# Kernel optimization log

Measured on AMD Instinct MI355X. Metric: run time of the kernel, lower is better.

Reference implementation:

```python
import jax, jax.numpy as jnp
import numpy as np

C = 512
GROUPS = 32
EPS = 1e-6

def setup_inputs() -> dict:
    key = jax.random.key(0)
    ks = jax.random.split(key, 8)
    b, h, w = 8, 64, 64
    s = 0.02
    return {
        "x": jax.random.normal(ks[0], (b, C, h, w), dtype=jnp.float32),
        "gn_gamma": jnp.ones((C,), jnp.float32),
        "gn_beta": jnp.zeros((C,), jnp.float32),
        "q_w": jax.random.normal(ks[1], (C, C), jnp.float32) * s,
        "q_b": jnp.zeros((C,), jnp.float32),
        "k_w": jax.random.normal(ks[2], (C, C), jnp.float32) * s,
        "k_b": jnp.zeros((C,), jnp.float32),
        "proj_w": jax.random.normal(ks[3], (C, C), jnp.float32) * s,
        "proj_b": jnp.zeros((C,), jnp.float32),
    }

def _group_norm(x, gamma, beta):
    b, c, h, w = x.shape
    xg = x.reshape(b, GROUPS, c // GROUPS, h, w)
    mu = jnp.mean(xg, axis=(2, 3, 4), keepdims=True)
    var = jnp.var(xg, axis=(2, 3, 4), keepdims=True)
    xn = ((xg - mu) * jax.lax.rsqrt(var + EPS)).reshape(b, c, h, w)
    return xn * gamma[None, :, None, None] + beta[None, :, None, None]

def _conv1x1(x, w, b):
    # x: (b,c,h,w), w: (out,in) -> (b,out,h,w)
    return jnp.einsum('bchw,oc->bohw', x, w) + b[None, :, None, None]

def reference(x, gn_gamma, gn_beta, q_w, q_b, k_w, k_b, proj_w, proj_b):
    b, c, h, w = x.shape
    r = _group_norm(x, gn_gamma, gn_beta)
    q = _conv1x1(r, q_w, q_b).reshape(b, c, h * w)   # (b,c,n)
    k = _conv1x1(r, k_w, k_b).reshape(b, c, h * w)   # (b,c,m)
    v = k  # faithful to source: v = self.k0(r)
    scale = jnp.asarray(c, x.dtype) ** -0.5
    scores = jnp.einsum('bcn,bcm->bnm', q, k) * scale  # (b,n,m)
    attn = jax.nn.softmax(scores, axis=-1)
    out = jnp.einsum('bcm,bnm->bcn', v, attn).reshape(b, c, h, w)
    out = _conv1x1(out, proj_w, proj_b)
    return x + out
```

## Files before the change

### kernel.cpp

```cpp
#include <hip/hip_runtime.h>
#include <hip/hip_bf16.h>
#include <cstdint>

#define DEVI __device__ __forceinline__

typedef __attribute__((ext_vector_type(8))) short short8;
typedef __attribute__((ext_vector_type(4))) float f32x4;
typedef unsigned int u32;
typedef unsigned short u16;

DEVI u16 f2bf(float f) {
  __hip_bfloat16 h = __float2bfloat16(f);
  return *reinterpret_cast<u16*>(&h);
}

DEVI void async_cp16(const __hip_bfloat16* g, __hip_bfloat16* l) {
  __builtin_amdgcn_global_load_lds(
      (const __attribute__((address_space(1))) u32*)(uintptr_t)g,
      (__attribute__((address_space(3))) u32*)(uintptr_t)l, 16, 0, 0);
}

DEVI void xcd_remap(int& bx, int& by, int& bz) {
  const int gx = gridDim.x, gy = gridDim.y;
  const int d = blockIdx.x + gx * (blockIdx.y + gridDim.y * blockIdx.z);
  const int idx = d >> 3;
  const int g = (d & 7) + 8 * (idx / gx);
  bx = idx % gx;
  by = g % gy;
  bz = g / gy;
}


template<int BIAS_MODE, bool EXPSUM>
__global__ __launch_bounds__(512, 2) void gemm256_tn(
    const __hip_bfloat16* __restrict__ A, int lda, size_t sA,
    const __hip_bfloat16* __restrict__ B, int ldb, size_t sB,
    void* __restrict__ Zv, int ldz, size_t sZ,
    const float* __restrict__ bias,
    float alpha, int K,
    float* __restrict__ rsum)
{
  __shared__ __hip_bfloat16 ls[3 * 16384];
  const int t  = threadIdx.x;
  const int bb = blockIdx.z;

  const int nbxy = gridDim.x * gridDim.y;
  const int borig = blockIdx.y * gridDim.x + blockIdx.x;
  const int cpx = nbxy >> 3;
  const int blog = (borig & 7) * cpx + (borig >> 3);
  const int bx = blog % gridDim.x;
  const int by = blog / gridDim.x;
  const int n0 = bx * 256;
  const int m0 = by * 256;

  const __hip_bfloat16* Ab = A + (size_t)bb * sA;
  const __hip_bfloat16* Bb = B + (size_t)bb * sB;

  const int lane = t & 63;
  const int quad = lane >> 4;
  const int l16  = lane & 15;
  const int wave = t >> 6;
  const int wm   = (wave >> 2) * 128;
  const int wn   = (wave & 3) * 64;
  const int qa   = (quad ^ (l16 & 3)) * 8;

  const int rowc = t >> 2;
  const int kc   = ((t & 3) ^ (rowc & 3)) * 8;
  const __hip_bfloat16* ga0 = Ab + (size_t)(m0 + rowc) * lda + kc;
  const __hip_bfloat16* ga1 = Ab + (size_t)(m0 + rowc + 128) * lda + kc;
  const __hip_bfloat16* gb0 = Bb + (size_t)(n0 + rowc) * ldb + kc;
  const __hip_bfloat16* gb1 = Bb + (size_t)(n0 + rowc + 128) * ldb + kc;

  f32x4 acc[8][4] = {};

#define STAGE256(SLOT)                                                        \
  {                                                                           \
    __hip_bfloat16* lb = ls + (SLOT) * 16384 + t * 8;                         \
    async_cp16(ga0, lb);                                                      \
    async_cp16(ga1, lb + 4096);                                               \
    async_cp16(gb0, lb + 8192);                                               \
    async_cp16(gb1, lb + 12288);                                              \
    ga0 += 32; ga1 += 32; gb0 += 32; gb1 += 32;                               \
  }

#define COMPUTE256(SLOT)                                                      \
  {                                                                           \
    const __hip_bfloat16* bA = ls + (SLOT) * 16384;                           \
    const __hip_bfloat16* bB = bA + 8192;                                     \
    short8 af[8], bfr[4];                                                     \
    _Pragma("unroll")                                                         \
    for (int i = 0; i < 8; ++i)                                               \
      af[i] = *(const short8*)(bA + (wm + i * 16 + l16) * 32 + qa);           \
    _Pragma("unroll")                                                         \
    for (int j = 0; j < 4; ++j)                                               \
      bfr[j] = *(const short8*)(bB + (wn + j * 16 + l16) * 32 + qa);          \
    _Pragma("unroll")                                                         \
    for (int i = 0; i < 8; ++i)                                               \
      _Pragma("unroll")                                                       \
      for (int j = 0; j < 4; ++j)                                             \
        acc[i][j] = __builtin_amdgcn_mfma_f32_16x16x32_bf16(af[i], bfr[j],    \
                                                            acc[i][j], 0, 0, 0); \
  }

  STAGE256(0);
  STAGE256(1);
  const int nk = K >> 5;
  for (int kw = 0; kw < nk - 1; ++kw) {
    asm volatile("s_waitcnt vmcnt(4)" ::: "memory");
    __builtin_amdgcn_s_barrier();
    if (kw + 2 < nk) {
      const int ss = (kw + 2) % 3;
      STAGE256(ss);
    }
    const int sc = kw % 3;
    COMPUTE256(sc);
  }
  asm volatile("s_waitcnt vmcnt(0)" ::: "memory");
  __builtin_amdgcn_s_barrier();
  COMPUTE256((nk - 1) % 3);

#undef STAGE256
#undef COMPUTE256

  if (EXPSUM) {
    __syncthreads();
    float* rs = (float*)ls;
    if (t < 256) rs[t] = 0.f;
    __syncthreads();
    float lsum[4] = {0.f, 0.f, 0.f, 0.f};
#pragma unroll
    for (int i = 0; i < 8; ++i) {
#pragma unroll
      for (int j = 0; j < 4; ++j) {
        const int m = m0 + wm + i * 16 + quad * 4;
        const int n = n0 + wn + j * 16 + l16;
        f32x4 v = acc[i][j];
        v[0] = __expf(v[0] * alpha); v[1] = __expf(v[1] * alpha);
        v[2] = __expf(v[2] * alpha); v[3] = __expf(v[3] * alpha);
        lsum[j] += v[0] + v[1] + v[2] + v[3];
        union { u16 s[4]; uint2 q; } pk;
        pk.s[0] = f2bf(v[0]); pk.s[1] = f2bf(v[1]);
        pk.s[2] = f2bf(v[2]); pk.s[3] = f2bf(v[3]);
        *(uint2*)((__hip_bfloat16*)Zv + (size_t)bb * sZ + (size_t)n * ldz + m) = pk.q;
      }
    }
#pragma unroll
    for (int j = 0; j < 4; ++j)
      atomicAdd(&rs[wn + j * 16 + l16], lsum[j]);
    __syncthreads();
    if (t < 256) atomicAdd(rsum + (size_t)bb * 4096 + n0 + t, rs[t]);
    return;
  }

#pragma unroll
  for (int i = 0; i < 8; ++i) {
#pragma unroll
    for (int j = 0; j < 4; ++j) {
      const int m = m0 + wm + i * 16 + quad * 4;
      const int n = n0 + wn + j * 16 + l16;
      f32x4 v = acc[i][j];
      if (BIAS_MODE == 1) v += *(const f32x4*)(bias + m);
      else if (BIAS_MODE == 2) v += bias[n];
      v *= alpha;
      union { u16 s[4]; uint2 q; } pk;
      pk.s[0] = f2bf(v[0]); pk.s[1] = f2bf(v[1]);
      pk.s[2] = f2bf(v[2]); pk.s[3] = f2bf(v[3]);
      *(uint2*)((__hip_bfloat16*)Zv + (size_t)bb * sZ + (size_t)n * ldz + m) = pk.q;
    }
  }
}

__global__ __launch_bounds__(512, 1) void gemm128x8w_final(
    const __hip_bfloat16* __restrict__ A, int lda, size_t sA,
    const __hip_bfloat16* __restrict__ B, int ldb, size_t sB,
    float* __restrict__ out, int ldz, size_t sZ,
    const float* __restrict__ bias,
    int K,
    const float* __restrict__ rsum,
    const float* __restrict__ xres)
{
  __shared__ __hip_bfloat16 ls[5 * 8192];
  const int t = threadIdx.x;

  int bx, by, bb;
  xcd_remap(bx, by, bb);
  const int n0 = bx * 128;
  const int m0 = by * 128;

  const __hip_bfloat16* Ab = A + (size_t)bb * sA;
  const __hip_bfloat16* Bb = B + (size_t)bb * sB;

  const int lane = t & 63;
  const int quad = lane >> 4;
  const int l16  = lane & 15;
  const int wave = t >> 6;
  const int wm   = (wave >> 2) * 64;
  const int wn   = (wave & 3) * 32;
  const int qa   = (quad ^ (l16 & 3)) * 8;

  const int rowc = t >> 2;
  const int kc   = ((t & 3) ^ (rowc & 3)) * 8;
  const __hip_bfloat16* ga0 = Ab + (size_t)(m0 + rowc) * lda + kc;
  const __hip_bfloat16* gb0 = Bb + (size_t)(n0 + rowc) * ldb + kc;

  f32x4 acc[4][2] = {};

#define STAGEPV(SLOT)                                                         \
  {                                                                           \
    __hip_bfloat16* lb = ls + (SLOT) * 8192 + t * 8;                          \
    async_cp16(ga0, lb);                                                      \
    async_cp16(gb0, lb + 4096);                                               \
    ga0 += 32; gb0 += 32;                                                     \
  }

#define COMPUTEPV(SLOT)                                                       \
  {                                                                           \
    const __hip_bfloat16* bA = ls + (SLOT) * 8192;                            \
    const __hip_bfloat16* bB = bA + 4096;                                     \
    short8 af[4], bfr[2];                                                     \
    _Pragma("unroll")                                                         \
    for (int i = 0; i < 4; ++i)                                               \
      af[i] = *(const short8*)(bA + (wm + i * 16 + l16) * 32 + qa);           \
    _Pragma("unroll")                                                         \
    for (int j = 0; j < 2; ++j)                                               \
      bfr[j] = *(const short8*)(bB + (wn + j * 16 + l16) * 32 + qa);          \
    _Pragma("unroll")                                                         \
    for (int i = 0; i < 4; ++i)                                               \
      _Pragma("unroll")                                                       \
      for (int j = 0; j < 2; ++j)                                             \
        acc[i][j] = __builtin_amdgcn_mfma_f32_16x16x32_bf16(af[i], bfr[j],    \
                                                            acc[i][j], 0, 0, 0); \
  }

  STAGEPV(0);
  STAGEPV(1);
  STAGEPV(2);
  STAGEPV(3);
  const int nk = K >> 5;
  for (int kw = 0; kw < nk - 4; ++kw) {
    asm volatile("s_waitcnt vmcnt(6)" ::: "memory");
    __builtin_amdgcn_s_barrier();
    STAGEPV((kw + 4) % 5);
    COMPUTEPV(kw % 5);
  }
  asm volatile("s_waitcnt vmcnt(6)" ::: "memory");
  __builtin_amdgcn_s_barrier();
  COMPUTEPV((nk - 4) % 5);
  asm volatile("s_waitcnt vmcnt(4)" ::: "memory");
  __builtin_amdgcn_s_barrier();
  COMPUTEPV((nk - 3) % 5);
  asm volatile("s_waitcnt vmcnt(2)" ::: "memory");
  __builtin_amdgcn_s_barrier();
  COMPUTEPV((nk - 2) % 5);
  asm volatile("s_waitcnt vmcnt(0)" ::: "memory");
  __builtin_amdgcn_s_barrier();
  COMPUTEPV((nk - 1) % 5);

#undef STAGEPV
#undef COMPUTEPV

#pragma unroll
  for (int i = 0; i < 4; ++i) {
#pragma unroll
    for (int j = 0; j < 2; ++j) {
      const int m = m0 + wm + i * 16 + quad * 4;
      const int n = n0 + wn + j * 16 + l16;
      f32x4 v = acc[i][j];
      const size_t zoff = (size_t)n * ldz + m;
      f32x4 rs = *(const f32x4*)(rsum + (size_t)bb * 4096 + m);
      f32x4 xx = *(const f32x4*)(xres + (size_t)bb * sZ + zoff);
      const float pbv = bias[n];
      v[0] = xx[0] + pbv + v[0] / rs[0];
      v[1] = xx[1] + pbv + v[1] / rs[1];
      v[2] = xx[2] + pbv + v[2] / rs[2];
      v[3] = xx[3] + pbv + v[3] / rs[3];
      *(f32x4*)(out + (size_t)bb * sZ + zoff) = v;
    }
  }
}

__global__ __launch_bounds__(256) void prep_stats(
    const float* __restrict__ qw, const float* __restrict__ kw,
    const float* __restrict__ pw, const float* __restrict__ qb,
    const float* __restrict__ kb,
    __hip_bfloat16* __restrict__ wqk, __hip_bfloat16* __restrict__ wp,
    float* __restrict__ bias_qk, float* __restrict__ rsum,
    const float* __restrict__ x, float2* __restrict__ stats) {
  const int blk = blockIdx.x;
  if (blk < 768) {
    const float* src = (blk < 256) ? qw : (blk < 512) ? kw : pw;
    __hip_bfloat16* dst = (blk < 256) ? wqk : (blk < 512) ? (wqk + 262144) : wp;
    const int i = ((blk & 255) * 256 + threadIdx.x) * 4;
    f32x4 v = *(const f32x4*)(src + i);
    union { u16 s4[4]; uint2 q; } pk;
    pk.s4[0] = f2bf(v[0]); pk.s4[1] = f2bf(v[1]);
    pk.s4[2] = f2bf(v[2]); pk.s4[3] = f2bf(v[3]);
    *(uint2*)(dst + i) = pk.q;
  } else if (blk == 768) {
    const int i = threadIdx.x * 4;
    *(f32x4*)(bias_qk + i) = *(const f32x4*)(qb + i);
    *(f32x4*)(bias_qk + 512 + i) = *(const f32x4*)(kb + i);
  } else if (blk < 801) {
    ((f32x4*)rsum)[(blk - 769) * 256 + threadIdx.x] = f32x4{0.f, 0.f, 0.f, 0.f};
  } else {
    const int bg = blk - 801;
    const f32x4* p = (const f32x4*)(x + (size_t)bg * 65536);
    float s = 0.f, s2 = 0.f;
    for (int i = threadIdx.x; i < 16384; i += 256) {
      f32x4 v = p[i];
      s  += v[0] + v[1] + v[2] + v[3];
      s2 += v[0]*v[0] + v[1]*v[1] + v[2]*v[2] + v[3]*v[3];
    }
    for (int o = 32; o > 0; o >>= 1) { s += __shfl_down(s, o); s2 += __shfl_down(s2, o); }
    __shared__ float wsum[4], wsum2[4];
    const int wave = threadIdx.x >> 6;
    if ((threadIdx.x & 63) == 0) { wsum[wave] = s; wsum2[wave] = s2; }
    __syncthreads();
    if (threadIdx.x == 0) {
      float S  = wsum[0] + wsum[1] + wsum[2] + wsum[3];
      float S2 = wsum2[0] + wsum2[1] + wsum2[2] + wsum2[3];
      float mu = S * (1.f / 65536.f);
      float var = S2 * (1.f / 65536.f) - mu * mu;
      stats[bg] = make_float2(mu, rsqrtf(var + 1e-6f));
    }
  }
}

__global__ __launch_bounds__(256) void gn_apply(const float* __restrict__ x,
                                                const float2* __restrict__ stats,
                                                const float* __restrict__ gamma,
                                                const float* __restrict__ beta,
                                                __hip_bfloat16* __restrict__ rt) {
  const int b = blockIdx.y, n0 = blockIdx.x * 64;
  __shared__ float tile[64][65];
  const int t  = threadIdx.x;
  const int cl = t >> 2;
  const int q4 = (t & 3) * 4;
  for (int cc = 0; cc < 8; ++cc) {
    const int c = cc * 64 + cl;
    const float2 ms = stats[b * 32 + (c >> 4)];
    const float ga = gamma[c] * ms.y;
    const float be = beta[c] - ms.x * ga;
    const float* src = x + ((size_t)b * 512 + c) * 4096 + n0;
#pragma unroll
    for (int p = 0; p < 4; ++p) {
      f32x4 v = *(const f32x4*)(src + q4 + p * 16);
      tile[cl][q4 + p * 16 + 0] = fmaf(v[0], ga, be);
      tile[cl][q4 + p * 16 + 1] = fmaf(v[1], ga, be);
      tile[cl][q4 + p * 16 + 2] = fmaf(v[2], ga, be);
      tile[cl][q4 + p * 16 + 3] = fmaf(v[3], ga, be);
    }
    __syncthreads();
    const int nw = t >> 2;
    const int cw = (t & 3) * 16;
    union { u16 s[16]; uint4 q[2]; } pk;
#pragma unroll
    for (int j = 0; j < 16; ++j) pk.s[j] = f2bf(tile[cw + j][nw]);
    __hip_bfloat16* dst = rt + ((size_t)b * 4096 + n0 + nw) * 512 + cc * 64 + cw;
    *(uint4*)dst = pk.q[0];
    *((uint4*)dst + 1) = pk.q[1];
    __syncthreads();
  }
}

extern "C" void kernel_launch(void* const* d_in, const int* in_sizes, int n_in,
                              void* d_out, int out_size, void* d_ws, size_t ws_size,
                              hipStream_t stream) {
  const float* x     = (const float*)d_in[0];
  const float* gamma = (const float*)d_in[1];
  const float* beta  = (const float*)d_in[2];
  const float* q_w   = (const float*)d_in[3];
  const float* q_b   = (const float*)d_in[4];
  const float* k_w   = (const float*)d_in[5];
  const float* k_b   = (const float*)d_in[6];
  const float* p_w   = (const float*)d_in[7];
  const float* p_b   = (const float*)d_in[8];
  float* out = (float*)d_out;

  constexpr int B = 8, C = 512, N = 4096;
  constexpr size_t NC = (size_t)N * C;
  constexpr size_t NN = (size_t)N * N;

  char* ws = (char*)d_ws;
  size_t off = 0;
  auto alloc = [&](size_t bytes) {
    void* p = ws + off;
    off += (bytes + 255) & ~(size_t)255;
    return p;
  };

  __hip_bfloat16* wqk = (__hip_bfloat16*)alloc((size_t)1024 * 512 * 2);
  __hip_bfloat16* wp  = (__hip_bfloat16*)alloc((size_t)C * C * 2);
  float* bias_qk      = (float*)alloc(1024 * 4);
  float2* stats       = (float2*)alloc((size_t)B * 32 * sizeof(float2));
  float* rsum         = (float*)alloc((size_t)B * N * 4);
  __hip_bfloat16* rt  = (__hip_bfloat16*)alloc(B * NC * 2);
  __hip_bfloat16* qkt = (__hip_bfloat16*)alloc(B * (size_t)N * 1024 * 2);
  __hip_bfloat16* wpv = (__hip_bfloat16*)alloc(B * NC * 2);
  const size_t base_off = off;

  const size_t attn_b_bytes = NN * 2;
  size_t avail = (ws_size > base_off) ? ws_size - base_off : 0;
  int G = 4;
  if (avail < 4 * attn_b_bytes) G = 2;
  if (avail < 2 * attn_b_bytes) G = 1;
  __hip_bfloat16* attn = (__hip_bfloat16*)alloc(attn_b_bytes * G);

  const dim3 blk(256);
  const dim3 blk512(512);
  const float scale = 0.044194173824159216f;

  prep_stats<<<dim3(801 + B * 32), blk, 0, stream>>>(
      q_w, k_w, p_w, q_b, k_b, wqk, wp, bias_qk, rsum, x, stats);

  gn_apply<<<dim3(64, B), blk, 0, stream>>>(x, stats, gamma, beta, rt);

  gemm256_tn<1, false><<<dim3(16, 4, B), blk512, 0, stream>>>(
      wqk, C, 0, rt, C, NC, qkt, 1024, (size_t)N * 1024,
      bias_qk, 1.f, C, nullptr);

  gemm256_tn<0, false><<<dim3(2, 16, B), blk512, 0, stream>>>(
      qkt + 512, 1024, (size_t)N * 1024, wp, C, 0,
      wpv, N, NC, nullptr, 1.f, C, nullptr);

  for (int b0 = 0; b0 < B; ) {
    const int Gc = (B - b0 < G) ? (B - b0) : G;

    gemm256_tn<0, true><<<dim3(16, 16, Gc), blk512, 0, stream>>>(
        qkt + (size_t)b0 * N * 1024 + 512, 1024, (size_t)N * 1024,
        qkt + (size_t)b0 * N * 1024,       1024, (size_t)N * 1024,
        attn, N, NN, nullptr, scale, C, rsum + (size_t)b0 * N);

    gemm128x8w_final<<<dim3(4, 32, Gc), blk512, 0, stream>>>(
        attn, N, NN, wpv + (size_t)b0 * NC, N, NC,
        out + (size_t)b0 * NC, N, NC, p_b, N,
        rsum + (size_t)b0 * N, x + (size_t)b0 * NC);

    b0 += Gc;
  }
}
```

Before: 676.0 us.

## Interleave async loads, LDS reads and MFMA phases with barriers and setprio

Splits the per-k-step GEMM compute into four MFMA phases, each preceded by one async global-to-LDS copy and a subset of LDS fragment reads. Barriers separate the phases, and s_setprio raises wave priority during MFMA bursts. The goal is to overlap memory traffic with matrix math and to keep waves' MFMA issue staggered, ping-pong style. The cost is four extra barriers per k-step, which may add sync overhead. The last-iteration special case is folded into the loop.

```diff
diff --git a/kernel.cpp b/kernel.cpp
--- a/kernel.cpp
+++ b/kernel.cpp
@@ -83,44 +83,62 @@
     ga0 += 32; ga1 += 32; gb0 += 32; gb1 += 32;                               \
   }
 
-#define COMPUTE256(SLOT)                                                      \
-  {                                                                           \
-    const __hip_bfloat16* bA = ls + (SLOT) * 16384;                           \
-    const __hip_bfloat16* bB = bA + 8192;                                     \
-    short8 af[8], bfr[4];                                                     \
-    _Pragma("unroll")                                                         \
-    for (int i = 0; i < 8; ++i)                                               \
-      af[i] = *(const short8*)(bA + (wm + i * 16 + l16) * 32 + qa);           \
-    _Pragma("unroll")                                                         \
-    for (int j = 0; j < 4; ++j)                                               \
-      bfr[j] = *(const short8*)(bB + (wn + j * 16 + l16) * 32 + qa);          \
-    _Pragma("unroll")                                                         \
-    for (int i = 0; i < 8; ++i)                                               \
+#define RD_AF(I0)                                                             \
+    _Pragma("unroll")                                                         \
+    for (int i = 0; i < 4; ++i)                                               \
+      af[(I0) + i] = *(const short8*)(bA + (wm + ((I0) + i) * 16 + l16) * 32 + qa);
+
+#define RD_BF(J0)                                                             \
+    _Pragma("unroll")                                                         \
+    for (int j = 0; j < 2; ++j)                                               \
+      bfr[(J0) + j] = *(const short8*)(bB + (wn + ((J0) + j) * 16 + l16) * 32 + qa);
+
+#define PH_MFMA(I0, J0)                                                       \
+    __builtin_amdgcn_s_setprio(1);                                            \
+    _Pragma("unroll")                                                         \
+    for (int i = 0; i < 4; ++i)                                               \
       _Pragma("unroll")                                                       \
-      for (int j = 0; j < 4; ++j)                                             \
-        acc[i][j] = __builtin_amdgcn_mfma_f32_16x16x32_bf16(af[i], bfr[j],    \
-                                                            acc[i][j], 0, 0, 0); \
-  }
+      for (int j = 0; j < 2; ++j)                                             \
+        acc[(I0) + i][(J0) + j] = __builtin_amdgcn_mfma_f32_16x16x32_bf16(    \
+            af[(I0) + i], bfr[(J0) + j], acc[(I0) + i][(J0) + j], 0, 0, 0);   \
+    __builtin_amdgcn_s_setprio(0);
 
   STAGE256(0);
   STAGE256(1);
   const int nk = K >> 5;
-  for (int kw = 0; kw < nk - 1; ++kw) {
-    asm volatile("s_waitcnt vmcnt(4)" ::: "memory");
-    __builtin_amdgcn_s_barrier();
-    if (kw + 2 < nk) {
-      const int ss = (kw + 2) % 3;
-      STAGE256(ss);
-    }
-    const int sc = kw % 3;
-    COMPUTE256(sc);
-  }
-  asm volatile("s_waitcnt vmcnt(0)" ::: "memory");
-  __builtin_amdgcn_s_barrier();
-  COMPUTE256((nk - 1) % 3);
+  for (int kw = 0; kw < nk; ++kw) {
+    if (kw == nk - 1) {
+      asm volatile("s_waitcnt vmcnt(0)" ::: "memory");
+    } else {
+      asm volatile("s_waitcnt vmcnt(4)" ::: "memory");
+    }
+    __builtin_amdgcn_s_barrier();
+    const __hip_bfloat16* bA = ls + (kw % 3) * 16384;
+    const __hip_bfloat16* bB = bA + 8192;
+    const bool st = (kw + 2 < nk);
+    __hip_bfloat16* lb = ls + ((kw + 2) % 3) * 16384 + t * 8;
+    short8 af[8], bfr[4];
+    if (st) { async_cp16(ga0, lb);         ga0 += 32; }
+    RD_AF(0); RD_BF(0);
+    __builtin_amdgcn_s_barrier();
+    PH_MFMA(0, 0);
+    if (st) { async_cp16(ga1, lb + 4096);  ga1 += 32; }
+    RD_BF(2);
+    __builtin_amdgcn_s_barrier();
+    PH_MFMA(0, 2);
+    if (st) { async_cp16(gb0, lb + 8192);  gb0 += 32; }
+    RD_AF(4);
+    __builtin_amdgcn_s_barrier();
+    PH_MFMA(4, 0);
+    if (st) { async_cp16(gb1, lb + 12288); gb1 += 32; }
+    __builtin_amdgcn_s_barrier();
+    PH_MFMA(4, 2);
+  }
 
 #undef STAGE256
-#undef COMPUTE256
+#undef RD_AF
+#undef RD_BF
+#undef PH_MFMA
 
   if (EXPSUM) {
     __syncthreads();
```

Measured after the change: 677.8 us. No clear change (+0.3%).
